# Optimization experiments

Measured on AMD Instinct MI355X. Metric: run time of the kernel, lower is better.

## Reference

```python
import jax, jax.numpy as jnp
import numpy as np

B, S, DM1, DM2, DK, DV = 8, 2048, 768, 768, 64, 64
EPS = 1e-5


def setup_inputs() -> dict:
    key = jax.random.key(0)
    ks = jax.random.split(key, 8)
    s1 = 1.0 / np.sqrt(DM1)
    s2 = 1.0 / np.sqrt(DM2)
    return {
        "x_1": jax.random.normal(ks[0], (B, S, DM1), jnp.float32),
        "x_2": jax.random.normal(ks[1], (B, S, DM2), jnp.float32),
        "Wq": jax.random.uniform(ks[2], (DM1, DK), jnp.float32, -s1, s1),
        "bq": jnp.zeros((DK,), jnp.float32),
        "Wk": jax.random.uniform(ks[3], (DM2, DK), jnp.float32, -s2, s2),
        "bk": jnp.zeros((DK,), jnp.float32),
        "Wv": jax.random.uniform(ks[4], (DM2, DV), jnp.float32, -s2, s2),
        "bv": jnp.zeros((DV,), jnp.float32),
        "gamma": jnp.ones((DV,), jnp.float32),
        "beta": jnp.zeros((DV,), jnp.float32),
    }


def reference(x_1, x_2, Wq, bq, Wk, bk, Wv, bv, gamma, beta):
    q = jnp.einsum("bsd,dk->bsk", x_1, Wq) + bq            # [B,S,DK]
    k = jnp.einsum("bsd,dk->bsk", x_2, Wk) + bk            # [B,S,DK]
    v = jnp.einsum("bsd,dv->bsv", x_2, Wv) + bv            # [B,S,DV]
    scores = jnp.einsum("bqk,bsk->bqs", q, k) / jnp.sqrt(jnp.float32(DK))
    w = jax.nn.softmax(scores, axis=-1)                    # [B,S,S]
    # reverse-weight transform (reverse=True)
    dim = w.shape[1]
    w = (1.0 - w) / (dim - 1)
    attn = jnp.einsum("bqs,bsv->bqv", w, v)                # [B,S,DV]
    mu = jnp.mean(attn, axis=-1, keepdims=True)
    var = jnp.var(attn, axis=-1, keepdims=True)
    out = (attn - mu) * jax.lax.rsqrt(var + EPS) * gamma + beta
    return out
```

## Files before the change

### kernel.cpp

```cpp
#include <hip/hip_runtime.h>
#include <hip/hip_bf16.h>

#define BATCH 8
#define SEQ   2048
#define DM    768
#define DD    64
#define BS (BATCH * SEQ)
#define SCALEQ 0.1803369380478f

typedef __bf16 bf16x8 __attribute__((ext_vector_type(8)));
typedef float  f32x4  __attribute__((ext_vector_type(4)));
typedef short  short8 __attribute__((ext_vector_type(8)));
typedef short  short4v __attribute__((ext_vector_type(4)));

#define MFMA16(a, b, c) __builtin_amdgcn_mfma_f32_16x16x32_bf16((a), (b), (c), 0, 0, 0)

__device__ __forceinline__ short f2bf(float x) {
    unsigned u = __builtin_bit_cast(unsigned, x);
    u = (u + 0x7fffu + ((u >> 16) & 1u)) >> 16;
    return (short)u;
}
__device__ __forceinline__ float bf2f(short s) {
    unsigned u = ((unsigned)(unsigned short)s) << 16;
    return __builtin_bit_cast(float, u);
}
__device__ __forceinline__ bf16x8 cvt8(float4 a, float4 b) {
    bf16x8 r;
    r[0] = (__bf16)a.x; r[1] = (__bf16)a.y; r[2] = (__bf16)a.z; r[3] = (__bf16)a.w;
    r[4] = (__bf16)b.x; r[5] = (__bf16)b.y; r[6] = (__bf16)b.z; r[7] = (__bf16)b.w;
    return r;
}

__global__ void prep_w_kernel(const float* __restrict__ Wq, const float* __restrict__ Wk,
                              const float* __restrict__ Wv, short* __restrict__ Wt,
                              float* __restrict__ C) {
    int idx = blockIdx.x * 256 + threadIdx.x;
    if (idx < BATCH * DD) C[idx] = 0.f;
    if (idx >= 3 * DM * DD) return;
    int m = idx / (DM * DD);
    int r = (idx % (DM * DD)) / DD;
    int c = idx % DD;
    const float* W = (m == 0) ? Wq : (m == 1) ? Wk : Wv;
    float scale = (m == 0) ? SCALEQ : 1.0f;
    Wt[m * DM * DD + c * DM + r] = f2bf(W[r * DD + c] * scale);
}

#define PHK 192
#define RSTR 200
__global__ __launch_bounds__(256) void proj_kernel(
        const float* __restrict__ x1, const float* __restrict__ x2,
        const short* __restrict__ Wt,
        const float* __restrict__ bq, const float* __restrict__ bk,
        const float* __restrict__ bv,
        short* __restrict__ Qs, short* __restrict__ Kb, short* __restrict__ Vtb,
        float* __restrict__ C) {
    __shared__ __align__(16) short wls[2][64 * RSTR];
    const int tid = threadIdx.x, wave = tid >> 6, lane = tid & 63;
    const int quad = lane >> 4, l15 = lane & 15;
    const int kv = blockIdx.x & 1;
    const int r0 = (blockIdx.x >> 1) * 64;
    const float* x = kv ? x2 : x1;
    const short* W0 = Wt + (kv ? (size_t)(DM * DD) : 0);
    const short* W1 = Wt + 2 * (size_t)(DM * DD);

    const int srow = tid >> 2;
    const int skseg = tid & 3;

    const float* xp = x + (size_t)(r0 + wave * 16 + l15) * DM + quad * 8;

    f32x4 acc0[4] = {}, acc1[4] = {};

    float4 cxa = *(const float4*)(xp);
    float4 cxb = *(const float4*)(xp + 4);

    for (int ph = 0; ph < 4; ph++) {
        const int kbase = ph * PHK;
#pragma unroll
        for (int i = 0; i < 6; i++) {
            int kp = skseg + 4 * i;
            bf16x8 w = *(const bf16x8*)(W0 + (size_t)srow * DM + kbase + kp * 8);
            *(bf16x8*)&wls[0][srow * RSTR + kp * 8] = w;
        }
        if (kv) {
#pragma unroll
            for (int i = 0; i < 6; i++) {
                int kp = skseg + 4 * i;
                bf16x8 w = *(const bf16x8*)(W1 + (size_t)srow * DM + kbase + kp * 8);
                *(bf16x8*)&wls[1][srow * RSTR + kp * 8] = w;
            }
        }
        __syncthreads();
#pragma unroll
        for (int st = 0; st < 6; st++) {
            const int k0 = kbase + st * 32;
            float4 nxa, nxb;
            if (k0 + 32 < DM) {
                nxa = *(const float4*)(xp + k0 + 32);
                nxb = *(const float4*)(xp + k0 + 36);
            }
            bf16x8 af = cvt8(cxa, cxb);
#pragma unroll
            for (int tn = 0; tn < 4; tn++) {
                const int lofs = (tn * 16 + l15) * RSTR + (st * 4 + quad) * 8;
                acc0[tn] = MFMA16(af, *(const bf16x8*)&wls[0][lofs], acc0[tn]);
                if (kv)
                    acc1[tn] = MFMA16(af, *(const bf16x8*)&wls[1][lofs], acc1[tn]);
            }
            cxa = nxa; cxb = nxb;
        }
        __syncthreads();
    }

    if (!kv) {
#pragma unroll
        for (int tn = 0; tn < 4; tn++) {
            int v = tn * 16 + l15;
            float bb = bq[v] * SCALEQ;
#pragma unroll
            for (int r = 0; r < 4; r++)
                Qs[(size_t)(r0 + wave * 16 + quad * 4 + r) * DD + v] = f2bf(acc0[tn][r] + bb);
        }
    } else {
#pragma unroll
        for (int tn = 0; tn < 4; tn++) {
            int v = tn * 16 + l15;
            float bb = bk[v];
#pragma unroll
            for (int r = 0; r < 4; r++)
                Kb[(size_t)(r0 + wave * 16 + quad * 4 + r) * DD + v] = f2bf(acc0[tn][r] + bb);
        }
        const int b = r0 / SEQ;
        const int sbase = (r0 % SEQ) + wave * 16 + quad * 4;
#pragma unroll
        for (int tn = 0; tn < 4; tn++) {
            int v = tn * 16 + l15;
            float bb = bv[v];
            short4v pk;
            float cs = 0.f;
#pragma unroll
            for (int r = 0; r < 4; r++) {
                pk[r] = f2bf(acc1[tn][r] + bb);
                cs += bf2f(pk[r]);
            }
            *(short4v*)(Vtb + ((size_t)b * DD + v) * SEQ + sbase) = pk;
            cs += __shfl_xor(cs, 16);
            cs += __shfl_xor(cs, 32);
            if (quad == 0) atomicAdd(&C[b * DD + v], cs);
        }
    }
}

#define PBS 72
__global__ __launch_bounds__(256, 2) void flash_kernel(
        const short* __restrict__ Q, const short* __restrict__ K,
        const short* __restrict__ Vt,
        short* __restrict__ Yp, float* __restrict__ Dp) {
    __shared__ __align__(16) short pbuf[4][64 * PBS];
    __shared__ float dl[4][64];
    const int tid  = threadIdx.x;
    const int wave = tid >> 6, lane = tid & 63, quad = lane >> 4, l15 = lane & 15;
    const int blk = blockIdx.x;
    const int b = blk & 7, qt = (blk >> 3) & 31, half = blk >> 8;
    const int q0 = qt * 64;

    bf16x8 qf[4][2];
#pragma unroll
    for (int qn = 0; qn < 4; qn++)
#pragma unroll
        for (int kc = 0; kc < 2; kc++)
            qf[qn][kc] = *(const bf16x8*)(Q + ((size_t)(b * SEQ + q0 + qn * 16 + l15)) * DD
                                          + kc * 32 + quad * 8);

    const short* Kbp = K  + (size_t)b * SEQ * DD;
    const short* Vbp = Vt + (size_t)b * DD * SEQ;
    f32x4 y[4][4] = {};
    float den[4] = {0.f, 0.f, 0.f, 0.f};
    short* pw = &pbuf[wave][0];

    const int s_begin = half * 1024 + wave * 256;
    for (int s0 = s_begin; s0 < s_begin + 256; s0 += 64) {
#pragma unroll
        for (int tn = 0; tn < 4; tn++) {
            const short* kf = Kbp + (size_t)(s0 + tn * 16 + l15) * DD + quad * 8;
            bf16x8 ka0 = *(const bf16x8*)kf;
            bf16x8 ka1 = *(const bf16x8*)(kf + 32);
#pragma unroll
            for (int qn = 0; qn < 4; qn++) {
                f32x4 z = {0.f, 0.f, 0.f, 0.f};
                z = MFMA16(ka0, qf[qn][0], z);
                z = MFMA16(ka1, qf[qn][1], z);
                short4v pk;
#pragma unroll
                for (int r = 0; r < 4; r++) {
                    float p = __builtin_amdgcn_exp2f(z[r]);
                    den[qn] += p;
                    pk[r] = f2bf(p);
                }
                *(short4v*)&pw[(qn * 16 + l15) * PBS + tn * 16 + quad * 4] = pk;
            }
        }
#pragma unroll
        for (int kc = 0; kc < 2; kc++) {
            bf16x8 pB[4];
#pragma unroll
            for (int qn = 0; qn < 4; qn++)
                pB[qn] = *(const bf16x8*)&pw[(qn * 16 + l15) * PBS + kc * 32 + quad * 8];
#pragma unroll
            for (int vn = 0; vn < 4; vn++) {
                bf16x8 va = *(const bf16x8*)(Vbp + (size_t)(vn * 16 + l15) * SEQ
                                             + s0 + kc * 32 + quad * 8);
#pragma unroll
                for (int qn = 0; qn < 4; qn++)
                    y[qn][vn] = MFMA16(va, pB[qn], y[qn][vn]);
            }
        }
    }
#pragma unroll
    for (int qn = 0; qn < 4; qn++) {
        den[qn] += __shfl_xor(den[qn], 16);
        den[qn] += __shfl_xor(den[qn], 32);
    }
#pragma unroll
    for (int qn = 0; qn < 4; qn++) {
#pragma unroll
        for (int vn = 0; vn < 4; vn++) {
            short4v pk;
#pragma unroll
            for (int r = 0; r < 4; r++) pk[r] = f2bf(y[qn][vn][r]);
            *(short4v*)&pw[(qn * 16 + l15) * PBS + vn * 16 + quad * 4] = pk;
        }
        if (quad == 0) dl[wave][qn * 16 + l15] = den[qn];
    }
    __syncthreads();
    {
        const int q = wave * 16 + l15;
        float D = dl[0][q] + dl[1][q] + dl[2][q] + dl[3][q];
        float ys[16];
#pragma unroll
        for (int j = 0; j < 16; j++) ys[j] = 0.f;
#pragma unroll
        for (int u = 0; u < 4; u++) {
#pragma unroll
            for (int h = 0; h < 2; h++) {
                bf16x8 t = *(const bf16x8*)&pbuf[u][q * PBS + quad * 16 + h * 8];
#pragma unroll
                for (int j = 0; j < 8; j++) ys[h * 8 + j] += (float)t[j];
            }
        }
        const size_t row = (size_t)b * SEQ + q0 + q;
        short8 o0, o1;
#pragma unroll
        for (int j = 0; j < 8; j++) { o0[j] = f2bf(ys[j]); o1[j] = f2bf(ys[8 + j]); }
        short* yout = Yp + ((size_t)half * BS + row) * DD + quad * 16;
        *(short8*)yout = o0;
        *(short8*)(yout + 8) = o1;
        if (quad == 0) Dp[half * BS + row] = D;
    }
}

__global__ __launch_bounds__(256) void reduce_ln_kernel(
        const short* __restrict__ Yp, const float* __restrict__ Dp,
        const float* __restrict__ C, const float* __restrict__ gamma,
        const float* __restrict__ beta, float* __restrict__ out) {
    const int row = blockIdx.x * 4 + (threadIdx.x >> 6);
    const int v = threadIdx.x & 63;
    const int b = row >> 11;
    float Y = bf2f(Yp[(size_t)row * DD + v]) + bf2f(Yp[((size_t)BS + row) * DD + v]);
    float D = Dp[row] + Dp[BS + row];
    float attn = (C[b * DD + v] - Y / D) * (1.0f / (float)(SEQ - 1));
    float msum = attn, ssum = attn * attn;
#pragma unroll
    for (int m = 1; m < 64; m <<= 1) {
        msum += __shfl_xor(msum, m);
        ssum += __shfl_xor(ssum, m);
    }
    float mu = msum * (1.0f / 64.0f);
    float var = ssum * (1.0f / 64.0f) - mu * mu;
    float rs = rsqrtf(var + 1e-5f);
    out[(size_t)row * DD + v] = (attn - mu) * rs * gamma[v] + beta[v];
}

extern "C" void kernel_launch(void* const* d_in, const int* in_sizes, int n_in,
                              void* d_out, int out_size, void* d_ws, size_t ws_size,
                              hipStream_t stream) {
    const float* x1    = (const float*)d_in[0];
    const float* x2    = (const float*)d_in[1];
    const float* Wq    = (const float*)d_in[2];
    const float* bq    = (const float*)d_in[3];
    const float* Wk    = (const float*)d_in[4];
    const float* bk    = (const float*)d_in[5];
    const float* Wv    = (const float*)d_in[6];
    const float* bv    = (const float*)d_in[7];
    const float* gamma = (const float*)d_in[8];
    const float* beta  = (const float*)d_in[9];
    float* out = (float*)d_out;

    char* ws = (char*)d_ws;
    short* Qs  = (short*)(ws);
    short* Kbf = (short*)(ws + (2ull << 20));
    short* Vtb = (short*)(ws + (4ull << 20));
    short* Wt  = (short*)(ws + (6ull << 20));
    float* Cc  = (float*)(ws + (6ull << 20) + 3 * DM * DD * 2);
    short* Yp  = (short*)(ws + (7ull << 20));
    float* Dp  = (float*)(ws + (11ull << 20));

    prep_w_kernel<<<576, 256, 0, stream>>>(Wq, Wk, Wv, Wt, Cc);
    proj_kernel<<<512, 256, 0, stream>>>(x1, x2, Wt, bq, bk, bv, Qs, Kbf, Vtb, Cc);
    flash_kernel<<<512, 256, 0, stream>>>(Qs, Kbf, Vtb, Yp, Dp);
    reduce_ln_kernel<<<BS / 4, 256, 0, stream>>>(Yp, Dp, Cc, gamma, beta, out);
}
```

Baseline: 171.1 us.

## Load projection weights via global_load_lds with XOR swizzle and deeper x prefetch

The projection kernel now stages weight tiles with direct global-to-LDS loads instead of going through registers. It uses an XOR-swizzled 64-wide layout in place of padded rows to avoid LDS bank conflicts. The x activations are prefetched a full phase ahead, six k-steps at a time. The trailing barrier is also replaced by a leading one, which removes one sync per phase but raises register pressure from the 12 float4 prefetch buffers.

```diff
diff --git a/kernel.cpp b/kernel.cpp
--- a/kernel.cpp
+++ b/kernel.cpp
@@ -29,6 +29,11 @@
     r[0] = (__bf16)a.x; r[1] = (__bf16)a.y; r[2] = (__bf16)a.z; r[3] = (__bf16)a.w;
     r[4] = (__bf16)b.x; r[5] = (__bf16)b.y; r[6] = (__bf16)b.z; r[7] = (__bf16)b.w;
     return r;
+}
+__device__ __forceinline__ void glds16(const void* g, void* l) {
+    __builtin_amdgcn_global_load_lds(
+        (const __attribute__((address_space(1))) void*)g,
+        (__attribute__((address_space(3))) void*)l, 16, 0, 0);
 }
 
 __global__ void prep_w_kernel(const float* __restrict__ Wq, const float* __restrict__ Wk,
@@ -46,7 +51,6 @@
 }
 
 #define PHK 192
-#define RSTR 200
 __global__ __launch_bounds__(256) void proj_kernel(
         const float* __restrict__ x1, const float* __restrict__ x2,
         const short* __restrict__ Wt,
@@ -54,7 +58,7 @@
         const float* __restrict__ bv,
         short* __restrict__ Qs, short* __restrict__ Kb, short* __restrict__ Vtb,
         float* __restrict__ C) {
-    __shared__ __align__(16) short wls[2][64 * RSTR];
+    __shared__ __align__(16) short wls[2][3][64 * 64];
     const int tid = threadIdx.x, wave = tid >> 6, lane = tid & 63;
     const int quad = lane >> 4, l15 = lane & 15;
     const int kv = blockIdx.x & 1;
@@ -63,52 +67,57 @@
     const short* W0 = Wt + (kv ? (size_t)(DM * DD) : 0);
     const short* W1 = Wt + 2 * (size_t)(DM * DD);
 
-    const int srow = tid >> 2;
-    const int skseg = tid & 3;
+    const int wrow = lane >> 3;
+    const int wslot = lane & 7;
 
     const float* xp = x + (size_t)(r0 + wave * 16 + l15) * DM + quad * 8;
 
     f32x4 acc0[4] = {}, acc1[4] = {};
 
-    float4 cxa = *(const float4*)(xp);
-    float4 cxb = *(const float4*)(xp + 4);
-
+    float4 xr[6][2];
+#pragma unroll
+    for (int st = 0; st < 6; st++) {
+        xr[st][0] = *(const float4*)(xp + st * 32);
+        xr[st][1] = *(const float4*)(xp + st * 32 + 4);
+    }
+
+#pragma unroll
     for (int ph = 0; ph < 4; ph++) {
         const int kbase = ph * PHK;
-#pragma unroll
-        for (int i = 0; i < 6; i++) {
-            int kp = skseg + 4 * i;
-            bf16x8 w = *(const bf16x8*)(W0 + (size_t)srow * DM + kbase + kp * 8);
-            *(bf16x8*)&wls[0][srow * RSTR + kp * 8] = w;
-        }
-        if (kv) {
-#pragma unroll
-            for (int i = 0; i < 6; i++) {
-                int kp = skseg + 4 * i;
-                bf16x8 w = *(const bf16x8*)(W1 + (size_t)srow * DM + kbase + kp * 8);
-                *(bf16x8*)&wls[1][srow * RSTR + kp * 8] = w;
+        if (ph) __syncthreads();
+#pragma unroll
+        for (int oct = 0; oct < 2; oct++) {
+            const int rbase = wave * 16 + oct * 8;
+            const short* s0 = W0 + (size_t)(rbase + wrow) * DM + kbase + (wslot ^ wrow) * 8;
+#pragma unroll
+            for (int g = 0; g < 3; g++)
+                glds16(s0 + g * 64, &wls[0][g][rbase * 64]);
+            if (kv) {
+                const short* s1 = W1 + (size_t)(rbase + wrow) * DM + kbase + (wslot ^ wrow) * 8;
+#pragma unroll
+                for (int g = 0; g < 3; g++)
+                    glds16(s1 + g * 64, &wls[1][g][rbase * 64]);
             }
         }
         __syncthreads();
 #pragma unroll
         for (int st = 0; st < 6; st++) {
-            const int k0 = kbase + st * 32;
-            float4 nxa, nxb;
-            if (k0 + 32 < DM) {
-                nxa = *(const float4*)(xp + k0 + 32);
-                nxb = *(const float4*)(xp + k0 + 36);
-            }
-            bf16x8 af = cvt8(cxa, cxb);
+            bf16x8 af = cvt8(
+                *(const float4*)&xr[st][0], *(const float4*)&xr[st][1]);
+            if (ph < 3) {
+                xr[st][0] = *(const float4*)(xp + kbase + PHK + st * 32);
+                xr[st][1] = *(const float4*)(xp + kbase + PHK + st * 32 + 4);
+            }
+            const int pg = st * 4 + quad, g = pg >> 3, q = pg & 7;
 #pragma unroll
             for (int tn = 0; tn < 4; tn++) {
-                const int lofs = (tn * 16 + l15) * RSTR + (st * 4 + quad) * 8;
-                acc0[tn] = MFMA16(af, *(const bf16x8*)&wls[0][lofs], acc0[tn]);
+                const int n = tn * 16 + l15;
+                const int lofs = n * 64 + (q ^ (n & 7)) * 8;
+                acc0[tn] = MFMA16(af, *(const bf16x8*)&wls[0][g][lofs], acc0[tn]);
                 if (kv)
-                    acc1[tn] = MFMA16(af, *(const bf16x8*)&wls[1][lofs], acc1[tn]);
-            }
-            cxa = nxa; cxb = nxb;
-        }
-        __syncthreads();
+                    acc1[tn] = MFMA16(af, *(const bf16x8*)&wls[1][g][lofs], acc1[tn]);
+            }
+        }
     }
 
     if (!kv) {
```

Result: no change. 171.7 us (+0.3%).

## Split projection into per-matrix blocks with full swizzled weight tile in LDS

Applied to the files above, without the earlier changes.

The projection kernel now launches one block per (row tile, matrix) instead of pairing K and V in one block, so x2 is read twice from global memory but the work is evenly balanced across blocks. Each block loads the whole 64x768 bf16 weight slice into LDS once, with an XOR swizzle to avoid bank conflicts, and drops the four-phase reload loop and its barriers. The grid grows from 512 to 768 blocks. In exchange the kernel uses 96KB of LDS per block with launch bounds set to one block per CU, which lowers occupancy and removes the software prefetch of x.

```diff
diff --git a/kernel.cpp b/kernel.cpp
--- a/kernel.cpp
+++ b/kernel.cpp
@@ -45,90 +45,68 @@
     Wt[m * DM * DD + c * DM + r] = f2bf(W[r * DD + c] * scale);
 }
 
-#define PHK 192
-#define RSTR 200
-__global__ __launch_bounds__(256) void proj_kernel(
+#define NGRP 12
+__global__ __launch_bounds__(256, 1) void proj_kernel(
         const float* __restrict__ x1, const float* __restrict__ x2,
         const short* __restrict__ Wt,
         const float* __restrict__ bq, const float* __restrict__ bk,
         const float* __restrict__ bv,
         short* __restrict__ Qs, short* __restrict__ Kb, short* __restrict__ Vtb,
         float* __restrict__ C) {
-    __shared__ __align__(16) short wls[2][64 * RSTR];
+    __shared__ __align__(16) short wls[NGRP][64 * 64];
     const int tid = threadIdx.x, wave = tid >> 6, lane = tid & 63;
     const int quad = lane >> 4, l15 = lane & 15;
-    const int kv = blockIdx.x & 1;
-    const int r0 = (blockIdx.x >> 1) * 64;
-    const float* x = kv ? x2 : x1;
-    const short* W0 = Wt + (kv ? (size_t)(DM * DD) : 0);
-    const short* W1 = Wt + 2 * (size_t)(DM * DD);
-
-    const int srow = tid >> 2;
-    const int skseg = tid & 3;
+    const int cls = blockIdx.x % 3;
+    const int r0 = (blockIdx.x / 3) * 64;
+    const float* x = (cls == 0) ? x1 : x2;
+    const short* W = Wt + (size_t)cls * DM * DD;
+
+    {
+        const int n = tid >> 2, kseg = tid & 3;
+#pragma unroll
+        for (int i = 0; i < 24; i++) {
+            const int p = kseg + i * 4;
+            bf16x8 w = *(const bf16x8*)(W + (size_t)n * DM + p * 8);
+            *(bf16x8*)&wls[p >> 3][n * 64 + ((p & 7) ^ (n & 7)) * 8] = w;
+        }
+    }
+    __syncthreads();
 
     const float* xp = x + (size_t)(r0 + wave * 16 + l15) * DM + quad * 8;
-
-    f32x4 acc0[4] = {}, acc1[4] = {};
-
-    float4 cxa = *(const float4*)(xp);
-    float4 cxb = *(const float4*)(xp + 4);
-
-    for (int ph = 0; ph < 4; ph++) {
-        const int kbase = ph * PHK;
-#pragma unroll
-        for (int i = 0; i < 6; i++) {
-            int kp = skseg + 4 * i;
-            bf16x8 w = *(const bf16x8*)(W0 + (size_t)srow * DM + kbase + kp * 8);
-            *(bf16x8*)&wls[0][srow * RSTR + kp * 8] = w;
-        }
-        if (kv) {
-#pragma unroll
-            for (int i = 0; i < 6; i++) {
-                int kp = skseg + 4 * i;
-                bf16x8 w = *(const bf16x8*)(W1 + (size_t)srow * DM + kbase + kp * 8);
-                *(bf16x8*)&wls[1][srow * RSTR + kp * 8] = w;
-            }
-        }
-        __syncthreads();
-#pragma unroll
-        for (int st = 0; st < 6; st++) {
-            const int k0 = kbase + st * 32;
-            float4 nxa, nxb;
-            if (k0 + 32 < DM) {
-                nxa = *(const float4*)(xp + k0 + 32);
-                nxb = *(const float4*)(xp + k0 + 36);
-            }
-            bf16x8 af = cvt8(cxa, cxb);
-#pragma unroll
-            for (int tn = 0; tn < 4; tn++) {
-                const int lofs = (tn * 16 + l15) * RSTR + (st * 4 + quad) * 8;
-                acc0[tn] = MFMA16(af, *(const bf16x8*)&wls[0][lofs], acc0[tn]);
-                if (kv)
-                    acc1[tn] = MFMA16(af, *(const bf16x8*)&wls[1][lofs], acc1[tn]);
-            }
-            cxa = nxa; cxb = nxb;
-        }
-        __syncthreads();
-    }
-
-    if (!kv) {
+    f32x4 acc[4] = {};
+#pragma unroll
+    for (int st = 0; st < 24; st++) {
+        float4 a = *(const float4*)(xp + st * 32);
+        float4 b = *(const float4*)(xp + st * 32 + 4);
+        bf16x8 af = cvt8(a, b);
+        const int p = st * 4 + quad, g = p >> 3, q = p & 7;
+#pragma unroll
+        for (int tn = 0; tn < 4; tn++) {
+            const int n = tn * 16 + l15;
+            acc[tn] = MFMA16(af, *(const bf16x8*)&wls[g][n * 64 + (q ^ (n & 7)) * 8],
+                             acc[tn]);
+        }
+    }
+
+    if (cls == 0) {
 #pragma unroll
         for (int tn = 0; tn < 4; tn++) {
             int v = tn * 16 + l15;
             float bb = bq[v] * SCALEQ;
 #pragma unroll
             for (int r = 0; r < 4; r++)
-                Qs[(size_t)(r0 + wave * 16 + quad * 4 + r) * DD + v] = f2bf(acc0[tn][r] + bb);
-        }
-    } else {
+                Qs[(size_t)(r0 + wave * 16 + quad * 4 + r) * DD + v] = f2bf(acc[tn][r] + bb);
+        }
+    } else if (cls == 1) {
 #pragma unroll
         for (int tn = 0; tn < 4; tn++) {
             int v = tn * 16 + l15;
             float bb = bk[v];
 #pragma unroll
             for (int r = 0; r < 4; r++)
-                Kb[(size_t)(r0 + wave * 16 + quad * 4 + r) * DD + v] = f2bf(acc0[tn][r] + bb);
-        }
+                Kb[(size_t)(r0 + wave * 16 + quad * 4 + r) * DD + v] = f2bf(acc[tn][r] + bb);
+        }
+    } else {
         const int b = r0 / SEQ;
         const int sbase = (r0 % SEQ) + wave * 16 + quad * 4;
 #pragma unroll
@@ -139,7 +117,7 @@
             float cs = 0.f;
 #pragma unroll
             for (int r = 0; r < 4; r++) {
-                pk[r] = f2bf(acc1[tn][r] + bb);
+                pk[r] = f2bf(acc[tn][r] + bb);
                 cs += bf2f(pk[r]);
             }
             *(short4v*)(Vtb + ((size_t)b * DD + v) * SEQ + sbase) = pk;
@@ -305,7 +283,7 @@
     float* Dp  = (float*)(ws + (11ull << 20));
 
     prep_w_kernel<<<576, 256, 0, stream>>>(Wq, Wk, Wv, Wt, Cc);
-    proj_kernel<<<512, 256, 0, stream>>>(x1, x2, Wt, bq, bk, bv, Qs, Kbf, Vtb, Cc);
+    proj_kernel<<<768, 256, 0, stream>>>(x1, x2, Wt, bq, bk, bv, Qs, Kbf, Vtb, Cc);
     flash_kernel<<<512, 256, 0, stream>>>(Qs, Kbf, Vtb, Yp, Dp);
     reduce_ln_kernel<<<BS / 4, 256, 0, stream>>>(Yp, Dp, Cc, gamma, beta, out);
 }
```

Result: slower. 203.0 us (+18.6%).
